# Kernel tuning notes

Hardware: AMD Instinct MI355X
Metric: run time of the kernel (lower is better)

The kernel has to match this reference:

```python
import jax, jax.numpy as jnp
import numpy as np

NUM_EMB = 8192
EMB_DIM = 64
TOP_K = 10
TEMP = 1.0
PERP_W = 0.01


def setup_inputs() -> dict:
    key = jax.random.key(0)
    k1, k2, k3 = jax.random.split(key, 3)
    inputs = jax.random.normal(k1, (8, 2048, EMB_DIM), dtype=jnp.float32)
    codebook = jax.random.normal(k2, (NUM_EMB, EMB_DIM), dtype=jnp.float32)
    # Gumbel noise for vectorized multinomial sampling over top-k (Gumbel-max trick)
    u = jax.random.uniform(k3, (8 * 2048, TOP_K), dtype=jnp.float32, minval=1e-6, maxval=1.0 - 1e-6)
    gumbel = -jnp.log(-jnp.log(u))
    return {"inputs": inputs, "codebook": codebook, "gumbel": gumbel}


def _vq_forward(inputs, codebook, gumbel):
    K, D = codebook.shape
    shp = inputs.shape
    flat = inputs.reshape(-1, D)                      # [N, D]
    valid = jnp.linalg.norm(flat, axis=1) > 1e-6      # [N]
    d = (jnp.sum(flat * flat, axis=1, keepdims=True)
         + jnp.sum(codebook * codebook, axis=1)
         - 2.0 * (flat @ codebook.T))
    # top-k smallest distances
    neg_top, top_idx = jax.lax.top_k(-d, TOP_K)       # [N, k]
    top_d = -neg_top
    logits = -top_d / TEMP
    # multinomial(softmax(logits)) sample per row via Gumbel-max (vectorized)
    j = jnp.argmax(logits + gumbel, axis=1)           # [N]
    rows = jnp.arange(flat.shape[0])
    idx = top_idx[rows, j]                            # sampled codebook indices [N]
    min_d = top_d[rows, j]                            # sampled distances [N]
    q_valid = codebook[idx]                           # embedding gather [N, D]
    vmask = valid[:, None].astype(flat.dtype)
    q_flat = q_valid * vmask                          # zero rows where invalid
    idx_flat = jnp.where(valid, idx, 0)
    min_d_flat = jnp.where(valid, min_d, jnp.zeros((), flat.dtype))
    n_valid = jnp.maximum(jnp.sum(valid.astype(flat.dtype)), 1.0)
    # codebook (VQ) loss: MSE over valid rows; commitment loss has 0 weight in source
    loss_vq = jnp.sum(vmask * (q_valid - jax.lax.stop_gradient(flat)) ** 2) / (n_valid * D)
    quantized = q_flat.reshape(shp)
    quantized_st = inputs + jax.lax.stop_gradient(quantized - inputs)
    # usage / perplexity from one-hot scatter-add over valid rows
    counts = jnp.zeros(K, dtype=flat.dtype).at[idx].add(valid.astype(flat.dtype))
    avg_probs = counts / n_valid
    perplexity = jnp.exp(-jnp.sum(avg_probs * jnp.log(avg_probs + 1e-10)))
    perplexity_loss = -jnp.log(perplexity + 1e-10)
    total_loss = loss_vq + PERP_W * perplexity_loss
    return quantized_st, total_loss, idx_flat, min_d_flat, perplexity


def reference(inputs, codebook, gumbel):
    return _vq_forward(inputs, codebook, gumbel)
```

## Files before the change

kernel.cpp:

```cpp
#include <hip/hip_runtime.h>
#include <hip/hip_bf16.h>

#define N_ROWS   16384
#define EMB_DIM  64
#define NUM_EMB  8192
#define TOP_K    10
#define PERP_W   0.01

#define M_CHUNK   12

#define QST_OFF   0
#define LOSS_OFF  (N_ROWS * EMB_DIM)
#define IDX_OFF   (LOSS_OFF + 1)
#define MIND_OFF  (IDX_OFF + N_ROWS)
#define PERP_OFF  (MIND_OFF + N_ROWS)

#define WS_E2C    0
#define WS_E2D    32768
#define WS_CBS    98304
#define WS_HIST   1146880
#define WS_LOSSP  1179648
#define WS_NVP    1212416
#define WS_C32    1228800

typedef short bf16x8 __attribute__((ext_vector_type(8)));
typedef float f32x4  __attribute__((ext_vector_type(4)));

__device__ __forceinline__ unsigned umx(unsigned a, unsigned b) {
    return __builtin_elementwise_max(a, b);
}
__device__ __forceinline__ unsigned umn(unsigned a, unsigned b) {
    return __builtin_elementwise_min(a, b);
}

__device__ __forceinline__ unsigned short f2bf(float f) {
    unsigned int u = __float_as_uint(f);
    unsigned int r = u + 0x7fffu + ((u >> 16) & 1u);
    return (unsigned short)(r >> 16);
}

__global__ __launch_bounds__(256) void vq_prep(const float* __restrict__ cb,
                                               float* __restrict__ e2c,
                                               double* __restrict__ e2d,
                                               unsigned short* __restrict__ cbs,
                                               int* __restrict__ hist) {
    const int k = blockIdx.x * 256 + threadIdx.x;
    hist[k] = 0;
    const float4* rp = (const float4*)(cb + (size_t)k * EMB_DIM);
    float  s  = 0.0f;
    double sd = 0.0;
    unsigned v32[32];
#pragma unroll
    for (int i = 0; i < 16; ++i) {
        const float4 v = rp[i];
        s += v.x * v.x + v.y * v.y + v.z * v.z + v.w * v.w;
        sd += (double)v.x * (double)v.x + (double)v.y * (double)v.y
            + (double)v.z * (double)v.z + (double)v.w * (double)v.w;
        v32[2 * i + 0] = (unsigned)f2bf(v.x) | ((unsigned)f2bf(v.y) << 16);
        v32[2 * i + 1] = (unsigned)f2bf(v.z) | ((unsigned)f2bf(v.w) << 16);
    }
    e2c[k] = 512.0f - 0.5f * s;
    e2d[k] = sd;

    const int tp   = k >> 5;
    const int r32  = k & 31;
    const int rsub = r32 & 15;
    unsigned short* basep = cbs + ((size_t)tp << 11)
                          + ((unsigned)(r32 & 16) << 6)
                          + (rsub << 3);
#pragma unroll
    for (int q2 = 0; q2 < 4; ++q2) {
        uint4 lo, hi;
        lo.x = v32[q2 * 4 + 0]; lo.y = v32[q2 * 4 + 1];
        lo.z = v32[q2 * 4 + 2]; lo.w = v32[q2 * 4 + 3];
        hi.x = v32[16 + q2 * 4 + 0]; hi.y = v32[16 + q2 * 4 + 1];
        hi.z = v32[16 + q2 * 4 + 2]; hi.w = v32[16 + q2 * 4 + 3];
        *(uint4*)(basep + q2 * 128)       = lo;
        *(uint4*)(basep + 512 + q2 * 128) = hi;
    }
}

__global__ __launch_bounds__(256) void vq_gemm_topk(
        const float* __restrict__ inp, const unsigned short* __restrict__ cbs,
        const float* __restrict__ e2c, unsigned short* __restrict__ cand32) {
    __shared__ unsigned keysh[16][193];

    const int tid   = threadIdx.x;
    const int w     = tid >> 6;
    const int lane  = tid & 63;
    const int q     = lane >> 4;
    const int rsub  = lane & 15;
    const int row0  = blockIdx.x * 16;
    const int row   = row0 + rsub;
    const int half0 = blockIdx.y * 4096;
    const int cbase = half0 + w * 1024;
    const int tpbase = cbase >> 5;

    const int eoff = q << 2;

    bf16x8 b0, b1;
    {
        const float* xp = inp + (size_t)row * EMB_DIM + q * 8;
#pragma unroll
        for (int j = 0; j < 8; ++j) b0[j] = (short)f2bf(xp[j]);
#pragma unroll
        for (int j = 0; j < 8; ++j) b1[j] = (short)f2bf(xp[32 + j]);
    }

    unsigned l0=0,l1=0,l2=0,l3=0,l4=0,l5=0,l6=0,l7=0,l8=0,l9=0,l10=0,l11=0;

#define LOADP(P0,P1,P2,P3,E0,E1,TT) { \
        const bf16x8* bp_ = ((const bf16x8*)cbs) + (size_t)(tpbase + (TT)) * 256; \
        P0 = bp_[lane];        P1 = bp_[lane + 64]; \
        P2 = bp_[lane + 128];  P3 = bp_[lane + 192]; \
        const float* ep_ = e2c + cbase + (TT) * 32; \
        E0 = *(const f32x4*)(ep_ + eoff); \
        E1 = *(const f32x4*)(ep_ + eoff + 16); }

    bf16x8 A00, A01, A10, A11, B00, B01, B10, B11;
    f32x4  Ae0, Ae1, Be0, Be1;
    LOADP(A00, A01, A10, A11, Ae0, Ae1, 0)
    LOADP(B00, B01, B10, B11, Be0, Be1, 1)

#define CE(A,B) { const unsigned mx_ = umx(A, B), mn_ = umn(A, B); \
                  A = mx_; B = mn_; }

#define SUBITER(P0,P1,P2,P3,E0,E1,TT,TP) { \
        const bf16x8 c00_ = P0, c01_ = P1, c10_ = P2, c11_ = P3; \
        const f32x4  ce0_ = E0, ce1_ = E1; \
        LOADP(P0, P1, P2, P3, E0, E1, (TP) & 31) \
        f32x4 acc0_ = __builtin_amdgcn_mfma_f32_16x16x32_bf16(c00_, b0, ce0_, 0, 0, 0); \
        acc0_       = __builtin_amdgcn_mfma_f32_16x16x32_bf16(c01_, b1, acc0_, 0, 0, 0); \
        f32x4 acc1_ = __builtin_amdgcn_mfma_f32_16x16x32_bf16(c10_, b0, ce1_, 0, 0, 0); \
        acc1_       = __builtin_amdgcn_mfma_f32_16x16x32_bf16(c11_, b1, acc1_, 0, 0, 0); \
        const unsigned tb_ = (unsigned)((TT) << 3); \
        unsigned k0 = (__float_as_uint(acc0_[0]) & 0xFFFFFF00u) | (tb_ + 0u); \
        unsigned k1 = (__float_as_uint(acc0_[1]) & 0xFFFFFF00u) | (tb_ + 1u); \
        unsigned k2 = (__float_as_uint(acc0_[2]) & 0xFFFFFF00u) | (tb_ + 2u); \
        unsigned k3 = (__float_as_uint(acc0_[3]) & 0xFFFFFF00u) | (tb_ + 3u); \
        unsigned k4 = (__float_as_uint(acc1_[0]) & 0xFFFFFF00u) | (tb_ + 4u); \
        unsigned k5 = (__float_as_uint(acc1_[1]) & 0xFFFFFF00u) | (tb_ + 5u); \
        unsigned k6 = (__float_as_uint(acc1_[2]) & 0xFFFFFF00u) | (tb_ + 6u); \
        unsigned k7 = (__float_as_uint(acc1_[3]) & 0xFFFFFF00u) | (tb_ + 7u); \
         \
        CE(k0,k1) CE(k2,k3) CE(k4,k5) CE(k6,k7) \
        CE(k0,k2) CE(k1,k3) CE(k4,k6) CE(k5,k7) \
        CE(k1,k2) CE(k5,k6) \
        CE(k0,k4) CE(k1,k5) CE(k2,k6) CE(k3,k7) \
        CE(k2,k4) CE(k3,k5) \
        CE(k1,k2) CE(k3,k4) CE(k5,k6) \
        if (k0 > l11) { \
             \
            CE(l11,k0) CE(l10,k1) CE(l9,k2) CE(l8,k3) \
            CE(l7,k4)  CE(l6,k5)  CE(l5,k6) CE(l4,k7) \
             \
            CE(l0,l6) CE(l1,l7) CE(l2,l8) CE(l3,l9) CE(l4,l10) CE(l5,l11) \
            CE(l0,l3) CE(l1,l4) CE(l2,l5) CE(l6,l9) CE(l7,l10) CE(l8,l11) \
            CE(l0,l1) CE(l0,l2) CE(l1,l2)  CE(l3,l4) CE(l3,l5) CE(l4,l5) \
            CE(l6,l7) CE(l6,l8) CE(l7,l8)  CE(l9,l10) CE(l9,l11) CE(l10,l11) \
        } }

    for (int t = 0; t < 32; t += 2) {
        SUBITER(A00, A01, A10, A11, Ae0, Ae1, t,     t + 2)
        SUBITER(B00, B01, B10, B11, Be0, Be1, t + 1, t + 3)
    }
#undef SUBITER
#undef CE
#undef LOADP

    {
        unsigned* kr = &keysh[rsub][w * 48 + q * 12];
        kr[0]=l0; kr[1]=l1; kr[2]=l2;  kr[3]=l3;
        kr[4]=l4; kr[5]=l5; kr[6]=l6;  kr[7]=l7;
        kr[8]=l8; kr[9]=l9; kr[10]=l10; kr[11]=l11;
    }
    __syncthreads();

    for (int rr = 0; rr < 4; ++rr) {
        const int lr = 4 * w + rr;
        const unsigned ka = keysh[lr][lane];
        const unsigned kb = keysh[lr][lane + 64];
        const unsigned kc = keysh[lr][lane + 128];

        unsigned tau = 0u;
#pragma unroll
        for (int b = 31; b >= 0; --b) {
            const unsigned t2 = tau | (1u << b);
            const int cnt = __popcll(__ballot(ka >= t2))
                          + __popcll(__ballot(kb >= t2))
                          + __popcll(__ballot(kc >= t2));
            if (cnt >= 16) tau = t2;
        }

        const unsigned long long m0 = __ballot(ka >= tau);
        const unsigned long long m1 = __ballot(kb >= tau);
        const unsigned long long m2 = __ballot(kc >= tau);
        const unsigned long long below = (lane == 0) ? 0ull
                                        : (~0ull >> (64 - lane));
        const int c0 = __popcll(m0);
        const int c1 = __popcll(m1);
        const int p0 = __popcll(m0 & below);
        const int p1 = c0 + __popcll(m1 & below);
        const int p2 = c0 + c1 + __popcll(m2 & below);

        unsigned short* outp =
            cand32 + (size_t)(row0 + lr) * 32 + blockIdx.y * 16;

#define EMIT(KX, SLOT, POS) \
        if ((KX) >= tau && (POS) < 16) { \
            const unsigned slot_ = (unsigned)(SLOT); \
            const unsigned idx_  = (KX) & 0xFFu; \
            const unsigned wq_   = slot_ / 48u; \
            const unsigned qq_   = (slot_ % 48u) / 12u; \
            const unsigned code_ = (unsigned)half0 + wq_ * 1024u \
                                 + ((idx_ >> 3) << 5) + (((idx_ >> 2) & 1u) << 4) \
                                 + (qq_ << 2) + (idx_ & 3u); \
            outp[POS] = (unsigned short)code_; \
        }
        EMIT(ka, lane,       p0)
        EMIT(kb, lane + 64,  p1)
        EMIT(kc, lane + 128, p2)
#undef EMIT
    }
}

__global__ __launch_bounds__(256) void vq_finalize(const float* __restrict__ inp,
                                                   const float* __restrict__ cb,
                                                   const double* __restrict__ e2d,
                                                   const float* __restrict__ gumbel,
                                                   const unsigned short* __restrict__ cand32,
                                                   float* __restrict__ out,
                                                   int* __restrict__ hist,
                                                   double* __restrict__ lossp,
                                                   int* __restrict__ nvp) {
    __shared__ double dvs[4][32];
    __shared__ int    dis[4][32];
    __shared__ double wl[4];
    __shared__ int    wv[4];

    const int tid  = threadIdx.x;
    const int w    = tid >> 6;
    const int lane = tid & 63;
    const int row  = blockIdx.x * 4 + w;
    const int g    = lane >> 2;
    const int lq   = lane & 3;

    const float xf = inp[(size_t)row * EMB_DIM + lane];
    const double xd = (double)xf;

    double x2 = xd * xd;
#pragma unroll
    for (int off = 32; off >= 1; off >>= 1) x2 += __shfl_xor(x2, off);
    const bool valid = sqrt(x2) > 1e-6;

    double xq[16];
    {
        const float4* xp = (const float4*)(inp + (size_t)row * EMB_DIM + (lq << 4));
#pragma unroll
        for (int i = 0; i < 4; ++i) {
            const float4 v = xp[i];
            xq[4 * i + 0] = (double)v.x; xq[4 * i + 1] = (double)v.y;
            xq[4 * i + 2] = (double)v.z; xq[4 * i + 3] = (double)v.w;
        }
    }

#pragma unroll
    for (int r = 0; r < 2; ++r) {
        const int j    = r * 16 + g;
        const int code = (int)cand32[(size_t)row * 32 + j];
        const float4* ep = (const float4*)(cb + ((size_t)code << 6) + (lq << 4));
        const float4 e0 = ep[0], e1 = ep[1], e2v = ep[2], e3 = ep[3];
        double d0 = 0.0, d1 = 0.0;
        d0 = fma(xq[0],  (double)e0.x, d0);  d0 = fma(xq[1],  (double)e0.y, d0);
        d0 = fma(xq[2],  (double)e0.z, d0);  d0 = fma(xq[3],  (double)e0.w, d0);
        d0 = fma(xq[4],  (double)e1.x, d0);  d0 = fma(xq[5],  (double)e1.y, d0);
        d0 = fma(xq[6],  (double)e1.z, d0);  d0 = fma(xq[7],  (double)e1.w, d0);
        d1 = fma(xq[8],  (double)e2v.x, d1); d1 = fma(xq[9],  (double)e2v.y, d1);
        d1 = fma(xq[10], (double)e2v.z, d1); d1 = fma(xq[11], (double)e2v.w, d1);
        d1 = fma(xq[12], (double)e3.x, d1);  d1 = fma(xq[13], (double)e3.y, d1);
        d1 = fma(xq[14], (double)e3.z, d1);  d1 = fma(xq[15], (double)e3.w, d1);
        double dot = d0 + d1;
        dot += __shfl_xor(dot, 1);
        dot += __shfl_xor(dot, 2);
        if (lq == 0) {
            dvs[w][j] = x2 + e2d[code] - 2.0 * dot;
            dis[w][j] = code;
        }
    }
    __syncthreads();

    const bool has = (lane < 32);
    double cd = has ? dvs[w][lane] : 1.0e300;
    int    ci = has ? dis[w][lane] : 0x7fffffff;

    int rank = 0;
#pragma unroll
    for (int off = 1; off < 32; ++off) {
        const double od = __shfl_xor(cd, off);
        const int    oi = __shfl_xor(ci, off);
        if (od < cd || (od == cd && oi < ci)) ++rank;
    }

    float sc = -3.0e38f;
    if (has && rank < TOP_K)
        sc = (float)(-cd) + gumbel[(size_t)row * TOP_K + rank];

    double bd = cd; int bi = ci; int brk = rank;
#pragma unroll
    for (int off = 1; off < 64; off <<= 1) {
        const float  os = __shfl_xor(sc, off);
        const double od = __shfl_xor(bd, off);
        const int    oi = __shfl_xor(bi, off);
        const int    ork = __shfl_xor(brk, off);
        if (os > sc || (os == sc && ork < brk)) {
            sc = os; bd = od; bi = oi; brk = ork;
        }
    }
    const int   cidx = bi;
    const float mind = (float)bd;

    const float vm = valid ? 1.0f : 0.0f;
    const float qv = cb[(size_t)cidx * EMB_DIM + lane];
    out[QST_OFF + (size_t)row * EMB_DIM + lane] = xf + (qv * vm - xf);

    const double dq = (double)qv - xd;
    double l = dq * dq * (double)vm;
#pragma unroll
    for (int off = 32; off >= 1; off >>= 1) l += __shfl_xor(l, off);

    if (lane == 0) {
        wl[w] = l;
        wv[w] = valid ? 1 : 0;
        if (valid) atomicAdd(&hist[cidx], 1);
        out[IDX_OFF + row]  = valid ? (float)cidx : 0.0f;
        out[MIND_OFF + row] = valid ? mind : 0.0f;
    }
    __syncthreads();
    if (tid == 0) {
        lossp[blockIdx.x] = wl[0] + wl[1] + wl[2] + wl[3];
        nvp[blockIdx.x]   = wv[0] + wv[1] + wv[2] + wv[3];
    }
}

__global__ __launch_bounds__(1024) void vq_scalars(const double* __restrict__ lossp,
                                                   const int* __restrict__ nvp,
                                                   const int* __restrict__ hist,
                                                   float* __restrict__ out) {
    __shared__ double red[1024];
    __shared__ double s_nv;
    const int tid = threadIdx.x;

    double lsum = 0.0;
    int    nvl  = 0;
#pragma unroll
    for (int i = 0; i < 4; ++i) {
        const int j = tid + 1024 * i;
        lsum += lossp[j];
        nvl  += nvp[j];
    }

    red[tid] = lsum;
    __syncthreads();
    for (int s = 512; s >= 1; s >>= 1) {
        if (tid < s) red[tid] += red[tid + s];
        __syncthreads();
    }
    const double losstot = red[0];
    __syncthreads();

    red[tid] = (double)nvl;
    __syncthreads();
    for (int s = 512; s >= 1; s >>= 1) {
        if (tid < s) red[tid] += red[tid + s];
        __syncthreads();
    }
    if (tid == 0) s_nv = (red[0] > 0.5) ? red[0] : 1.0;
    __syncthreads();
    const double nv = s_nv;
    __syncthreads();

    double h = 0.0;
#pragma unroll
    for (int i = 0; i < 8; ++i) {
        const int k = tid + 1024 * i;
        const double p = (double)hist[k] / nv;
        h += p * log(p + 1e-10);
    }
    red[tid] = h;
    __syncthreads();
    for (int s = 512; s >= 1; s >>= 1) {
        if (tid < s) red[tid] += red[tid + s];
        __syncthreads();
    }
    if (tid == 0) {
        const double H = red[0];
        const double perp = exp(-H);
        const double ploss = -log(perp + 1e-10);
        const double lvq = losstot / (nv * (double)EMB_DIM);
        out[LOSS_OFF] = (float)(lvq + PERP_W * ploss);
        out[PERP_OFF] = (float)perp;
    }
}

extern "C" void kernel_launch(void* const* d_in, const int* in_sizes, int n_in,
                              void* d_out, int out_size, void* d_ws, size_t ws_size,
                              hipStream_t stream) {
    const float* inp    = (const float*)d_in[0];
    const float* cb     = (const float*)d_in[1];
    const float* gumbel = (const float*)d_in[2];
    float* out = (float*)d_out;

    char* ws = (char*)d_ws;
    float*          e2c    = (float*)(ws + WS_E2C);
    double*         e2d    = (double*)(ws + WS_E2D);
    unsigned short* cbs    = (unsigned short*)(ws + WS_CBS);
    int*            hist   = (int*)(ws + WS_HIST);
    double*         lossp  = (double*)(ws + WS_LOSSP);
    int*            nvp    = (int*)(ws + WS_NVP);
    unsigned short* cand32 = (unsigned short*)(ws + WS_C32);

    vq_prep<<<NUM_EMB / 256, 256, 0, stream>>>(cb, e2c, e2d, cbs, hist);
    vq_gemm_topk<<<dim3(N_ROWS / 16, 2), 256, 0, stream>>>(inp, cbs, e2c, cand32);
    vq_finalize<<<N_ROWS / 4, 256, 0, stream>>>(inp, cb, e2d, gumbel, cand32, out,
                                                hist, lossp, nvp);
    vq_scalars<<<1, 1024, 0, stream>>>(lossp, nvp, hist, out);
}
```

Measured before the change: 188.1 us.

## Fuse scalar reduction into finalize via last-block pattern; widen prep parallelism

```diff
diff --git a/kernel.cpp b/kernel.cpp
--- a/kernel.cpp
+++ b/kernel.cpp
@@ -19,9 +19,10 @@
 #define WS_E2D    32768
 #define WS_CBS    98304
 #define WS_HIST   1146880
-#define WS_LOSSP  1179648
-#define WS_NVP    1212416
-#define WS_C32    1228800
+#define WS_LP64   1179648
+#define WS_NV64   1183744
+#define WS_DONE   1187840
+#define WS_C32    1187904
 
 typedef short bf16x8 __attribute__((ext_vector_type(8)));
 typedef float f32x4  __attribute__((ext_vector_type(4)));
@@ -43,41 +44,46 @@
                                                float* __restrict__ e2c,
                                                double* __restrict__ e2d,
                                                unsigned short* __restrict__ cbs,
-                                               int* __restrict__ hist) {
-    const int k = blockIdx.x * 256 + threadIdx.x;
-    hist[k] = 0;
-    const float4* rp = (const float4*)(cb + (size_t)k * EMB_DIM);
+                                               int* __restrict__ hist,
+                                               double* __restrict__ lp64,
+                                               int* __restrict__ nv64,
+                                               int* __restrict__ done) {
+    const int g  = blockIdx.x * 256 + threadIdx.x;
+    const int k  = g >> 2;
+    const int lq = g & 3;
+
+    if (g < NUM_EMB) hist[g] = 0;
+    if (g < 64) { lp64[g * 8] = 0.0; nv64[g * 16] = 0; }
+    if (g == 0) *done = 0;
+
+    const float4* rp = (const float4*)(cb + (size_t)k * EMB_DIM + lq * 16);
     float  s  = 0.0f;
     double sd = 0.0;
-    unsigned v32[32];
-#pragma unroll
-    for (int i = 0; i < 16; ++i) {
+    unsigned pk[8];
+#pragma unroll
+    for (int i = 0; i < 4; ++i) {
         const float4 v = rp[i];
-        s += v.x * v.x + v.y * v.y + v.z * v.z + v.w * v.w;
+        s  += v.x * v.x + v.y * v.y + v.z * v.z + v.w * v.w;
         sd += (double)v.x * (double)v.x + (double)v.y * (double)v.y
             + (double)v.z * (double)v.z + (double)v.w * (double)v.w;
-        v32[2 * i + 0] = (unsigned)f2bf(v.x) | ((unsigned)f2bf(v.y) << 16);
-        v32[2 * i + 1] = (unsigned)f2bf(v.z) | ((unsigned)f2bf(v.w) << 16);
-    }
-    e2c[k] = 512.0f - 0.5f * s;
-    e2d[k] = sd;
-
-    const int tp   = k >> 5;
-    const int r32  = k & 31;
-    const int rsub = r32 & 15;
+        pk[2 * i + 0] = (unsigned)f2bf(v.x) | ((unsigned)f2bf(v.y) << 16);
+        pk[2 * i + 1] = (unsigned)f2bf(v.z) | ((unsigned)f2bf(v.w) << 16);
+    }
+    s  += __shfl_xor(s, 1);  s  += __shfl_xor(s, 2);
+    sd += __shfl_xor(sd, 1); sd += __shfl_xor(sd, 2);
+    if (lq == 0) { e2c[k] = 512.0f - 0.5f * s; e2d[k] = sd; }
+
+    const int tp = k >> 5, r32 = k & 31, rsub = r32 & 15;
     unsigned short* basep = cbs + ((size_t)tp << 11)
                           + ((unsigned)(r32 & 16) << 6)
                           + (rsub << 3);
-#pragma unroll
-    for (int q2 = 0; q2 < 4; ++q2) {
-        uint4 lo, hi;
-        lo.x = v32[q2 * 4 + 0]; lo.y = v32[q2 * 4 + 1];
-        lo.z = v32[q2 * 4 + 2]; lo.w = v32[q2 * 4 + 3];
-        hi.x = v32[16 + q2 * 4 + 0]; hi.y = v32[16 + q2 * 4 + 1];
-        hi.z = v32[16 + q2 * 4 + 2]; hi.w = v32[16 + q2 * 4 + 3];
-        *(uint4*)(basep + q2 * 128)       = lo;
-        *(uint4*)(basep + 512 + q2 * 128) = hi;
-    }
+    const int hi  = lq >> 1;
+    const int q2s = (lq & 1) * 2;
+    uint4 c0, c1;
+    c0.x = pk[0]; c0.y = pk[1]; c0.z = pk[2]; c0.w = pk[3];
+    c1.x = pk[4]; c1.y = pk[5]; c1.z = pk[6]; c1.w = pk[7];
+    *(uint4*)(basep + hi * 512 + (q2s + 0) * 128) = c0;
+    *(uint4*)(basep + hi * 512 + (q2s + 1) * 128) = c1;
 }
 
 __global__ __launch_bounds__(256) void vq_gemm_topk(
@@ -231,12 +237,16 @@
                                                    const unsigned short* __restrict__ cand32,
                                                    float* __restrict__ out,
                                                    int* __restrict__ hist,
-                                                   double* __restrict__ lossp,
-                                                   int* __restrict__ nvp) {
+                                                   double* __restrict__ lp64,
+                                                   int* __restrict__ nv64,
+                                                   int* __restrict__ done) {
     __shared__ double dvs[4][32];
     __shared__ int    dis[4][32];
     __shared__ double wl[4];
     __shared__ int    wv[4];
+    __shared__ double red[256];
+    __shared__ double s_nv;
+    __shared__ int    s_last;
 
     const int tid  = threadIdx.x;
     const int w    = tid >> 6;
@@ -248,6 +258,15 @@
     const float xf = inp[(size_t)row * EMB_DIM + lane];
     const double xd = (double)xf;
 
+    const int code0 = (int)cand32[(size_t)row * 32 + g];
+    const int code1 = (int)cand32[(size_t)row * 32 + 16 + g];
+    const float4* ep0 = (const float4*)(cb + ((size_t)code0 << 6) + (lq << 4));
+    const float4* ep1 = (const float4*)(cb + ((size_t)code1 << 6) + (lq << 4));
+    const float4 a0 = ep0[0], a1 = ep0[1], a2 = ep0[2], a3 = ep0[3];
+    const float4 b0 = ep1[0], b1 = ep1[1], b2 = ep1[2], b3 = ep1[3];
+    const double ed0 = e2d[code0];
+    const double ed1 = e2d[code1];
+
     double x2 = xd * xd;
 #pragma unroll
     for (int off = 32; off >= 1; off >>= 1) x2 += __shfl_xor(x2, off);
@@ -264,29 +283,27 @@
         }
     }
 
-#pragma unroll
-    for (int r = 0; r < 2; ++r) {
-        const int j    = r * 16 + g;
-        const int code = (int)cand32[(size_t)row * 32 + j];
-        const float4* ep = (const float4*)(cb + ((size_t)code << 6) + (lq << 4));
-        const float4 e0 = ep[0], e1 = ep[1], e2v = ep[2], e3 = ep[3];
-        double d0 = 0.0, d1 = 0.0;
-        d0 = fma(xq[0],  (double)e0.x, d0);  d0 = fma(xq[1],  (double)e0.y, d0);
-        d0 = fma(xq[2],  (double)e0.z, d0);  d0 = fma(xq[3],  (double)e0.w, d0);
-        d0 = fma(xq[4],  (double)e1.x, d0);  d0 = fma(xq[5],  (double)e1.y, d0);
-        d0 = fma(xq[6],  (double)e1.z, d0);  d0 = fma(xq[7],  (double)e1.w, d0);
-        d1 = fma(xq[8],  (double)e2v.x, d1); d1 = fma(xq[9],  (double)e2v.y, d1);
-        d1 = fma(xq[10], (double)e2v.z, d1); d1 = fma(xq[11], (double)e2v.w, d1);
-        d1 = fma(xq[12], (double)e3.x, d1);  d1 = fma(xq[13], (double)e3.y, d1);
-        d1 = fma(xq[14], (double)e3.z, d1);  d1 = fma(xq[15], (double)e3.w, d1);
-        double dot = d0 + d1;
-        dot += __shfl_xor(dot, 1);
-        dot += __shfl_xor(dot, 2);
-        if (lq == 0) {
-            dvs[w][j] = x2 + e2d[code] - 2.0 * dot;
-            dis[w][j] = code;
-        }
-    }
+#define DOT16(V0,V1,V2,V3, EDV, J) { \
+        double d0_ = 0.0, d1_ = 0.0; \
+        d0_ = fma(xq[0],  (double)V0.x, d0_);  d0_ = fma(xq[1],  (double)V0.y, d0_); \
+        d0_ = fma(xq[2],  (double)V0.z, d0_);  d0_ = fma(xq[3],  (double)V0.w, d0_); \
+        d0_ = fma(xq[4],  (double)V1.x, d0_);  d0_ = fma(xq[5],  (double)V1.y, d0_); \
+        d0_ = fma(xq[6],  (double)V1.z, d0_);  d0_ = fma(xq[7],  (double)V1.w, d0_); \
+        d1_ = fma(xq[8],  (double)V2.x, d1_);  d1_ = fma(xq[9],  (double)V2.y, d1_); \
+        d1_ = fma(xq[10], (double)V2.z, d1_);  d1_ = fma(xq[11], (double)V2.w, d1_); \
+        d1_ = fma(xq[12], (double)V3.x, d1_);  d1_ = fma(xq[13], (double)V3.y, d1_); \
+        d1_ = fma(xq[14], (double)V3.z, d1_);  d1_ = fma(xq[15], (double)V3.w, d1_); \
+        double dot_ = d0_ + d1_; \
+        dot_ += __shfl_xor(dot_, 1); \
+        dot_ += __shfl_xor(dot_, 2); \
+        if (lq == 0) { \
+            dvs[w][J] = x2 + (EDV) - 2.0 * dot_; \
+            dis[w][J] = (J) < 16 ? code0 : code1; \
+        } }
+
+    DOT16(a0, a1, a2, a3, ed0, g)
+    DOT16(b0, b1, b2, b3, ed1, 16 + g)
+#undef DOT16
     __syncthreads();
 
     const bool has = (lane < 32);
@@ -336,69 +353,63 @@
         out[MIND_OFF + row] = valid ? mind : 0.0f;
     }
     __syncthreads();
+
     if (tid == 0) {
-        lossp[blockIdx.x] = wl[0] + wl[1] + wl[2] + wl[3];
-        nvp[blockIdx.x]   = wv[0] + wv[1] + wv[2] + wv[3];
-    }
-}
-
-__global__ __launch_bounds__(1024) void vq_scalars(const double* __restrict__ lossp,
-                                                   const int* __restrict__ nvp,
-                                                   const int* __restrict__ hist,
-                                                   float* __restrict__ out) {
-    __shared__ double red[1024];
-    __shared__ double s_nv;
-    const int tid = threadIdx.x;
-
-    double lsum = 0.0;
-    int    nvl  = 0;
-#pragma unroll
-    for (int i = 0; i < 4; ++i) {
-        const int j = tid + 1024 * i;
-        lsum += lossp[j];
-        nvl  += nvp[j];
-    }
-
-    red[tid] = lsum;
+        const int slot = (int)(blockIdx.x & 63);
+        atomicAdd(&lp64[slot * 8], wl[0] + wl[1] + wl[2] + wl[3]);
+        atomicAdd(&nv64[slot * 16], wv[0] + wv[1] + wv[2] + wv[3]);
+        __threadfence();
+        const int old = atomicAdd(done, 1);
+        s_last = (old == (int)gridDim.x - 1) ? 1 : 0;
+    }
     __syncthreads();
-    for (int s = 512; s >= 1; s >>= 1) {
-        if (tid < s) red[tid] += red[tid + s];
-        __syncthreads();
-    }
-    const double losstot = red[0];
-    __syncthreads();
-
-    red[tid] = (double)nvl;
-    __syncthreads();
-    for (int s = 512; s >= 1; s >>= 1) {
-        if (tid < s) red[tid] += red[tid + s];
-        __syncthreads();
-    }
-    if (tid == 0) s_nv = (red[0] > 0.5) ? red[0] : 1.0;
-    __syncthreads();
-    const double nv = s_nv;
-    __syncthreads();
-
-    double h = 0.0;
-#pragma unroll
-    for (int i = 0; i < 8; ++i) {
-        const int k = tid + 1024 * i;
-        const double p = (double)hist[k] / nv;
-        h += p * log(p + 1e-10);
-    }
-    red[tid] = h;
-    __syncthreads();
-    for (int s = 512; s >= 1; s >>= 1) {
-        if (tid < s) red[tid] += red[tid + s];
-        __syncthreads();
-    }
-    if (tid == 0) {
-        const double H = red[0];
-        const double perp = exp(-H);
-        const double ploss = -log(perp + 1e-10);
-        const double lvq = losstot / (nv * (double)EMB_DIM);
-        out[LOSS_OFF] = (float)(lvq + PERP_W * ploss);
-        out[PERP_OFF] = (float)perp;
+
+    if (s_last) {
+        double lsum = 0.0; int nvl = 0;
+        if (tid < 64) {
+            lsum = atomicAdd(&lp64[tid * 8], 0.0);
+            nvl  = atomicAdd(&nv64[tid * 16], 0);
+        }
+        red[tid] = lsum;
+        __syncthreads();
+        for (int s = 128; s >= 1; s >>= 1) {
+            if (tid < s) red[tid] += red[tid + s];
+            __syncthreads();
+        }
+        const double losstot = red[0];
+        __syncthreads();
+
+        red[tid] = (double)nvl;
+        __syncthreads();
+        for (int s = 128; s >= 1; s >>= 1) {
+            if (tid < s) red[tid] += red[tid + s];
+            __syncthreads();
+        }
+        if (tid == 0) s_nv = (red[0] > 0.5) ? red[0] : 1.0;
+        __syncthreads();
+        const double nv = s_nv;
+        __syncthreads();
+
+        double h = 0.0;
+        for (int k = tid; k < NUM_EMB; k += 256) {
+            const int c = atomicAdd(&hist[k], 0);
+            const double p = (double)c / nv;
+            h += p * log(p + 1e-10);
+        }
+        red[tid] = h;
+        __syncthreads();
+        for (int s = 128; s >= 1; s >>= 1) {
+            if (tid < s) red[tid] += red[tid + s];
+            __syncthreads();
+        }
+        if (tid == 0) {
+            const double H = red[0];
+            const double perp = exp(-H);
+            const double ploss = -log(perp + 1e-10);
+            const double lvq = losstot / (nv * (double)EMB_DIM);
+            out[LOSS_OFF] = (float)(lvq + PERP_W * ploss);
+            out[PERP_OFF] = (float)perp;
+        }
     }
 }
 
@@ -415,13 +426,14 @@
     double*         e2d    = (double*)(ws + WS_E2D);
     unsigned short* cbs    = (unsigned short*)(ws + WS_CBS);
     int*            hist   = (int*)(ws + WS_HIST);
-    double*         lossp  = (double*)(ws + WS_LOSSP);
-    int*            nvp    = (int*)(ws + WS_NVP);
+    double*         lp64   = (double*)(ws + WS_LP64);
+    int*            nv64   = (int*)(ws + WS_NV64);
+    int*            done   = (int*)(ws + WS_DONE);
     unsigned short* cand32 = (unsigned short*)(ws + WS_C32);
 
-    vq_prep<<<NUM_EMB / 256, 256, 0, stream>>>(cb, e2c, e2d, cbs, hist);
+    vq_prep<<<NUM_EMB * 4 / 256, 256, 0, stream>>>(cb, e2c, e2d, cbs, hist,
+                                                   lp64, nv64, done);
     vq_gemm_topk<<<dim3(N_ROWS / 16, 2), 256, 0, stream>>>(inp, cbs, e2c, cand32);
     vq_finalize<<<N_ROWS / 4, 256, 0, stream>>>(inp, cb, e2d, gumbel, cand32, out,
-                                                hist, lossp, nvp);
-    vq_scalars<<<1, 1024, 0, stream>>>(lossp, nvp, hist, out);
-}
+                                                hist, lp64, nv64, done);
+}
```

Measured after the change: 272.3 us. 1.45x slower.
